# Kernel optimization log

Measured on AMD Instinct MI355X. Metric: run time of the kernel, lower is better.

## Reference

```python
import jax, jax.numpy as jnp
import numpy as np

N = 8192
E = 262144
IN_DIM = 128
OUT_DIM = 16


def _linear_params(key, fan_in, fan_out):
    k1, k2 = jax.random.split(key)
    bound = 1.0 / np.sqrt(fan_in)
    W = jax.random.uniform(k1, (fan_in, fan_out), jnp.float32, -bound, bound)
    b = jax.random.uniform(k2, (fan_out,), jnp.float32, -bound, bound)
    return W, b


def setup_inputs() -> dict:
    key = jax.random.key(0)
    ks = jax.random.split(key, 10)
    x = jax.random.normal(ks[0], (N, IN_DIM), jnp.float32)
    edge_index = jax.random.randint(ks[1], (2, E), 0, N, jnp.int64)
    W1, b1 = _linear_params(ks[2], IN_DIM, 128)
    W2, b2 = _linear_params(ks[3], 128, 256)
    W3, b3 = _linear_params(ks[4], 256, 64)
    Wk, bk = _linear_params(ks[5], 256, 256)
    Wq, bq = _linear_params(ks[6], 256, 256)
    Wr, br = _linear_params(ks[7], IN_DIM, 64)
    Wf, bf = _linear_params(ks[8], 64, OUT_DIM)
    ln_g = jnp.ones((64,), jnp.float32)
    ln_b = jnp.zeros((64,), jnp.float32)
    return dict(x=x, edge_index=edge_index, W1=W1, b1=b1, W2=W2, b2=b2,
                W3=W3, b3=b3, Wk=Wk, bk=bk, Wq=Wq, bq=bq, Wr=Wr, br=br,
                ln_g=ln_g, ln_b=ln_b, Wf=Wf, bf=bf)


def gcn_conv(x, W, b, row, col, n):
    # PyG GCNConv: add self-loops, symmetric normalization, aggregate src->dst
    xw = x @ W                                          # [N, F_out]
    loops = jnp.arange(n, dtype=row.dtype)
    r = jnp.concatenate([row, loops])
    c = jnp.concatenate([col, loops])
    deg = jax.ops.segment_sum(jnp.ones_like(c, jnp.float32), c, num_segments=n)
    dinv = jnp.where(deg > 0, jax.lax.rsqrt(jnp.maximum(deg, 1e-12)), 0.0)
    norm = dinv[r] * dinv[c]                            # [E+N]
    out = jax.ops.segment_sum(norm[:, None] * xw[r], c, num_segments=n)
    return out + b


def _forward(x, edge_index, W1, b1, W2, b2, W3, b3, Wk, bk, Wq, bq,
             Wr, br, ln_g, ln_b, Wf, bf):
    row, col = edge_index[0], edge_index[1]
    n = x.shape[0]
    residual = x @ Wr + br                              # [N, 64]
    h = jax.nn.leaky_relu(gcn_conv(x, W1, b1, row, col, n))   # dropout = eval no-op
    h = jax.nn.leaky_relu(gcn_conv(h, W2, b2, row, col, n))   # [N, 256]
    keys = h @ Wk + bk
    queries = h @ Wq + bq
    scores = queries @ keys.T                           # [N, N] dense, as in source
    mask = jnp.zeros((n, n), jnp.float32).at[row, col].set(1.0)
    scores = scores * mask                              # multiplicative mask (faithful)
    attn = jax.nn.softmax(scores, axis=-1)
    h = attn @ h                                        # [N, 256]
    h = jax.nn.leaky_relu(gcn_conv(h, W3, b3, row, col, n))   # [N, 64]
    z = h + residual
    mu = jnp.mean(z, axis=-1, keepdims=True)
    var = jnp.mean((z - mu) ** 2, axis=-1, keepdims=True)
    z = (z - mu) * jax.lax.rsqrt(var + 1e-5) * ln_g + ln_b
    pooled = jnp.max(z, axis=0)                         # 'max' pooling -> [64]
    return pooled @ Wf + bf                             # [OUT_DIM]


def reference(x, edge_index, W1, b1, W2, b2, W3, b3, Wk, bk, Wq, bq,
              Wr, br, ln_g, ln_b, Wf, bf):
    return _forward(x, edge_index, W1, b1, W2, b2, W3, b3, Wk, bk, Wq, bq,
                    Wr, br, ln_g, ln_b, Wf, bf)
```

## Files before the change

kernel.cpp:

```cpp
#include <hip/hip_runtime.h>
#include <hip/hip_fp16.h>
#include <cstdint>
#include <cstddef>

#define NNODES 8192
#define NEDGES 262144
#define MAXDEG 96
#define SMEM_BYTES 10496

typedef _Float16 f16x8 __attribute__((ext_vector_type(8)));
typedef _Float16 h2v   __attribute__((ext_vector_type(2)));
typedef float    f32x4 __attribute__((ext_vector_type(4)));

__device__ __forceinline__ float leaky(float v){ return v > 0.f ? v : 0.01f*v; }

__device__ __forceinline__ unsigned fmap(float f){
  unsigned u = __float_as_uint(f);
  return (u & 0x80000000u) ? ~u : (u | 0x80000000u);
}
__device__ __forceinline__ float funmap(unsigned u){
  return (u & 0x80000000u) ? __uint_as_float(u & 0x7FFFFFFFu) : __uint_as_float(~u);
}
__device__ __forceinline__ h2v as_h2(unsigned u){
  union{ unsigned x; h2v h; } c; c.x = u; return c.h;
}

struct GP {
  const float *x; const int *ei;
  const float *W1,*b1,*W2,*b2,*W3,*b3,*Wk,*bk,*Wq,*bq,*Wr,*br,*lng,*lnb,*Wf,*bfv;
  float* out;
  __half *xw1h,*h1h,*h1ah,*h2h,*qth,*gh,*hw3h;
  float *resid,*sw3;
  __half *Wqkt,*W2t,*W3t;
  float *bqk,*wb,*s0p;
  int *degc,*degr,*csrc,*csrd;
  unsigned* poolpart;
};

__device__ __forceinline__ void gemm_tile(const __half* __restrict__ A,
    const __half* __restrict__ Bt, const float* __restrict__ bias,
    float* __restrict__ Cf, __half* __restrict__ Ch, float* __restrict__ csum,
    int K, int N, int act, int bx, int by,
    _Float16 (*As)[40], _Float16 (*Bs)[40], float* cs){
  int t = threadIdx.x, w = t>>6, lane = t&63;
  int m0 = bx*64, n0 = by*64;
  int quad = lane>>4, l15 = lane&15;
  int srow = t>>2, soff = (t&3)*8;
  f32x4 acc0 = {0.f,0.f,0.f,0.f}, acc1 = acc0, acc2 = acc0, acc3 = acc0;
  for (int k0 = 0; k0 < K; k0 += 32){
    *(uint4*)&As[srow][soff] = *(const uint4*)(A  + (size_t)(m0+srow)*K + k0 + soff);
    *(uint4*)&Bs[srow][soff] = *(const uint4*)(Bt + (size_t)(n0+srow)*K + k0 + soff);
    __syncthreads();
    f16x8 af = *(const f16x8*)&As[w*16 + l15][quad*8];
    f16x8 b0 = *(const f16x8*)&Bs[ 0 + l15][quad*8];
    f16x8 b1 = *(const f16x8*)&Bs[16 + l15][quad*8];
    f16x8 b2 = *(const f16x8*)&Bs[32 + l15][quad*8];
    f16x8 b3 = *(const f16x8*)&Bs[48 + l15][quad*8];
    acc0 = __builtin_amdgcn_mfma_f32_16x16x32_f16(af, b0, acc0, 0,0,0);
    acc1 = __builtin_amdgcn_mfma_f32_16x16x32_f16(af, b1, acc1, 0,0,0);
    acc2 = __builtin_amdgcn_mfma_f32_16x16x32_f16(af, b2, acc2, 0,0,0);
    acc3 = __builtin_amdgcn_mfma_f32_16x16x32_f16(af, b3, acc3, 0,0,0);
    __syncthreads();
  }
  f32x4 accs[4] = {acc0, acc1, acc2, acc3};
  if (csum){
    if (t < 64) cs[t] = 0.f;
    __syncthreads();
    #pragma unroll
    for (int nt=0; nt<4; ++nt){
      float pp = accs[nt][0]+accs[nt][1]+accs[nt][2]+accs[nt][3];
      atomicAdd(&cs[nt*16 + l15], pp);
    }
    __syncthreads();
    if (t < 64) atomicAdd(&csum[n0 + t], cs[t]);
  }
  #pragma unroll
  for (int nt=0; nt<4; ++nt){
    int col = n0 + nt*16 + l15;
    float bv = bias ? bias[col] : 0.f;
    #pragma unroll
    for (int r=0;r<4;r++){
      int row = m0 + w*16 + quad*4 + r;
      float v = accs[nt][r] + bv;
      if (act) v = leaky(v);
      if (Cf) Cf[(size_t)row*N + col] = v;
      if (Ch) Ch[(size_t)row*N + col] = __float2half(v);
    }
  }
}

template<int TRANSB>
__device__ __forceinline__ void gemm_f32(const float* __restrict__ A,
    const float* __restrict__ B, const float* __restrict__ bias,
    float* __restrict__ Cf, __half* __restrict__ Ch,
    int K, int N, int bx, int by,
    _Float16 (*As)[40], _Float16 (*Bs)[40]){
  int t = threadIdx.x, w = t>>6, lane = t&63;
  int m0 = bx*64, n0 = by*64;
  int quad = lane>>4, l15 = lane&15;
  int srow = t>>2, soff = (t&3)*8;
  f32x4 acc0 = {0.f,0.f,0.f,0.f}, acc1 = acc0, acc2 = acc0, acc3 = acc0;
  for (int k0 = 0; k0 < K; k0 += 32){
    float4 a0 = *(const float4*)(A + (size_t)(m0+srow)*K + k0 + soff);
    float4 a1 = *(const float4*)(A + (size_t)(m0+srow)*K + k0 + soff + 4);
    _Float16* ad = &As[srow][soff];
    ad[0]=(_Float16)a0.x; ad[1]=(_Float16)a0.y; ad[2]=(_Float16)a0.z; ad[3]=(_Float16)a0.w;
    ad[4]=(_Float16)a1.x; ad[5]=(_Float16)a1.y; ad[6]=(_Float16)a1.z; ad[7]=(_Float16)a1.w;
    _Float16* bd = &Bs[srow][soff];
    if (TRANSB){
      #pragma unroll
      for (int u=0;u<8;u++)
        bd[u] = (_Float16)B[(size_t)(k0+soff+u)*N + n0+srow];
    } else {
      float4 b0 = *(const float4*)(B + (size_t)(n0+srow)*K + k0 + soff);
      float4 b1 = *(const float4*)(B + (size_t)(n0+srow)*K + k0 + soff + 4);
      bd[0]=(_Float16)b0.x; bd[1]=(_Float16)b0.y; bd[2]=(_Float16)b0.z; bd[3]=(_Float16)b0.w;
      bd[4]=(_Float16)b1.x; bd[5]=(_Float16)b1.y; bd[6]=(_Float16)b1.z; bd[7]=(_Float16)b1.w;
    }
    __syncthreads();
    f16x8 af = *(const f16x8*)&As[w*16 + l15][quad*8];
    f16x8 b0 = *(const f16x8*)&Bs[ 0 + l15][quad*8];
    f16x8 b1 = *(const f16x8*)&Bs[16 + l15][quad*8];
    f16x8 b2 = *(const f16x8*)&Bs[32 + l15][quad*8];
    f16x8 b3 = *(const f16x8*)&Bs[48 + l15][quad*8];
    acc0 = __builtin_amdgcn_mfma_f32_16x16x32_f16(af, b0, acc0, 0,0,0);
    acc1 = __builtin_amdgcn_mfma_f32_16x16x32_f16(af, b1, acc1, 0,0,0);
    acc2 = __builtin_amdgcn_mfma_f32_16x16x32_f16(af, b2, acc2, 0,0,0);
    acc3 = __builtin_amdgcn_mfma_f32_16x16x32_f16(af, b3, acc3, 0,0,0);
    __syncthreads();
  }
  f32x4 accs[4] = {acc0, acc1, acc2, acc3};
  #pragma unroll
  for (int nt=0; nt<4; ++nt){
    int col = n0 + nt*16 + l15;
    float bv = bias ? bias[col] : 0.f;
    #pragma unroll
    for (int r=0;r<4;r++){
      int row = m0 + w*16 + quad*4 + r;
      float v = accs[nt][r] + bv;
      if (Cf) Cf[(size_t)row*N + col] = v;
      if (Ch) Ch[(size_t)row*N + col] = __float2half(v);
    }
  }
}

template<int INS, int OUTS, int ACT>
__device__ __forceinline__ void agg128w(const __half* __restrict__ in,
    const int* __restrict__ deg, const int* __restrict__ src,
    __half* __restrict__ outp, const float* __restrict__ bias, int i){
  int lane = threadIdx.x & 63;
  int dcc = deg[i];
  float dc = rsqrtf((float)(dcc+1));
  int e0 = i*MAXDEG, e1 = e0 + dcc;
  float2 acc = make_float2(0.f, 0.f);
  for (int eb = e0; eb < e1; eb += 8){
    int m = e1 - eb; if (m > 8) m = 8;
    int r[8];
    #pragma unroll
    for (int u=0;u<8;u++) r[u] = src[(u<m) ? eb+u : eb];
    __half2 hv[8]; float sc[8];
    #pragma unroll
    for (int u=0;u<8;u++){
      hv[u] = *(const __half2*)(in + (size_t)r[u]*128 + lane*2);
      sc[u] = INS ? 1.f : rsqrtf((float)(deg[r[u]]+1));
    }
    #pragma unroll
    for (int u=0;u<8;u++){
      if (u < m){
        float2 h = __half22float2(hv[u]);
        if (INS){ acc.x += h.x; acc.y += h.y; }
        else { acc.x = fmaf(sc[u], h.x, acc.x); acc.y = fmaf(sc[u], h.y, acc.y); }
      }
    }
  }
  float2 self = __half22float2(*(const __half2*)(in + (size_t)i*128 + lane*2));
  float ss = INS ? 1.f : dc;
  float ox = dc*(ss*self.x + acc.x);
  float oy = dc*(ss*self.y + acc.y);
  if (ACT){
    ox = leaky(ox + bias[lane*2]);
    oy = leaky(oy + bias[lane*2+1]);
  }
  if (OUTS){ ox *= dc; oy *= dc; }
  *(__half2*)(outp + (size_t)i*128 + lane*2) = __floats2half2_rn(ox, oy);
}

__device__ __forceinline__ void attn_unit(const GP& p, int u){
  const int n = NNODES;
  int w = threadIdx.x>>6, lane = threadIdx.x&63;
  int i = u*4 + w;
  int fo = lane*4;
  uint2 qtu = *(const uint2*)(p.qth + (size_t)i*256 + fo);
  h2v q0 = as_h2(qtu.x), q1 = as_h2(qtu.y);
  float4 wbv = *(const float4*)(p.wb + fo);
  uint2 hiu  = *(const uint2*)(p.h2h + (size_t)i*256 + fo);
  float2 hia = __half22float2(*(__half2*)&hiu.x);
  float2 hib = __half22float2(*(__half2*)&hiu.y);
  float pv = hia.x*wbv.x + hia.y*wbv.y + hib.x*wbv.z + hib.y*wbv.w;
  #pragma unroll
  for (int mm=32; mm; mm>>=1) pv += __shfl_xor(pv, mm, 64);
  float base = pv + p.s0p[0];
  int dri = p.degr[i];
  int e0 = i*MAXDEG, e1 = e0 + dri;
  float acc = 0.f, dsum = 0.f;
  int slot = lane & 7;
  for (int eb = e0; eb < e1; eb += 8){
    int m = e1 - eb; if (m > 8) m = 8;
    int j[8];
    #pragma unroll
    for (int u8=0;u8<8;u8++) j[u8] = p.csrd[(u8<m) ? eb+u8 : eb];
    uint2 hv[8]; float gv[8];
    #pragma unroll
    for (int u8=0;u8<8;u8++){
      hv[u8] = *(const uint2*)(p.h2h + (size_t)j[u8]*256 + fo);
      gv[u8] = __half2float(p.gh[(size_t)j[u8]*64 + lane]);
    }
    float d[8];
    #pragma unroll
    for (int u8=0;u8<8;u8++)
      d[u8] = __builtin_amdgcn_fdot2(q1, as_h2(hv[u8].y),
              __builtin_amdgcn_fdot2(q0, as_h2(hv[u8].x), 0.f, false), false);
    #pragma unroll
    for (int v=0;v<8;v++) d[v] += __shfl_xor(d[v], 1, 64);
    float e0_ = (lane&1) ? d[1] : d[0];
    float e1_ = (lane&1) ? d[3] : d[2];
    float e2_ = (lane&1) ? d[5] : d[4];
    float e3_ = (lane&1) ? d[7] : d[6];
    e0_ += __shfl_xor(e0_, 2, 64);  e1_ += __shfl_xor(e1_, 2, 64);
    e2_ += __shfl_xor(e2_, 2, 64);  e3_ += __shfl_xor(e3_, 2, 64);
    float f0_ = (lane&2) ? e1_ : e0_;
    float f1_ = (lane&2) ? e3_ : e2_;
    f0_ += __shfl_xor(f0_, 4, 64);  f1_ += __shfl_xor(f1_, 4, 64);
    float g_ = (lane&4) ? f1_ : f0_;
    g_ += __shfl_xor(g_,  8, 64);
    g_ += __shfl_xor(g_, 16, 64);
    g_ += __shfl_xor(g_, 32, 64);
    float wep = __expf(g_ + base);
    float wm = (slot < m) ? wep : 0.f;
    wm += __shfl_xor(wm, 1, 64);
    wm += __shfl_xor(wm, 2, 64);
    wm += __shfl_xor(wm, 4, 64);
    dsum += wm;
    #pragma unroll
    for (int u8=0;u8<8;u8++){
      if (u8 < m){
        float wu = __shfl(wep, u8, 64);
        acc = fmaf(wu - 1.f, gv[u8], acc);
      }
    }
  }
  float inv = 1.0f / ((float)(n - dri) + dsum);
  float di = rsqrtf((float)(p.degc[i]+1));
  p.hw3h[(size_t)i*64 + lane] = __float2half(di * (p.sw3[lane] + acc) * inv);
}

__device__ __forceinline__ void zp_wave(const GP& p, int c){
  int lane = threadIdx.x & 63;
  int dcc = p.degc[c];
  float dc = rsqrtf((float)(dcc+1));
  float acc = 0.f;
  int e0 = c*MAXDEG, e1 = e0 + dcc;
  for (int eb = e0; eb < e1; eb += 8){
    int m = e1 - eb; if (m > 8) m = 8;
    int r[8];
    #pragma unroll
    for (int u=0;u<8;u++) r[u] = p.csrc[(u<m) ? eb+u : eb];
    __half hval[8];
    #pragma unroll
    for (int u=0;u<8;u++) hval[u] = p.hw3h[(size_t)r[u]*64 + lane];
    #pragma unroll
    for (int u=0;u<8;u++)
      if (u < m) acc += __half2float(hval[u]);
  }
  float self = __half2float(p.hw3h[(size_t)c*64 + lane]);
  float v = leaky(dc*(self + acc) + p.b3[lane]) + p.resid[(size_t)c*64 + lane];
  float s = v;
  #pragma unroll
  for (int mm=32; mm; mm>>=1) s += __shfl_xor(s, mm, 64);
  float mu = s * (1.0f/64.0f);
  float d = v - mu;
  float s2 = d*d;
  #pragma unroll
  for (int mm=32; mm; mm>>=1) s2 += __shfl_xor(s2, mm, 64);
  float zv = d * rsqrtf(s2*(1.0f/64.0f) + 1e-5f) * p.lng[lane] + p.lnb[lane];
  atomicMax(&p.poolpart[(c & 63)*64 + lane], fmap(zv));
}

__device__ __forceinline__ void final_unit(const GP& p, char* smem){
  int t = threadIdx.x, f = t & 63, g = t >> 6;
  unsigned (*sm)[64] = (unsigned(*)[64])smem;
  float* pool = (float*)(smem + 1024);
  unsigned mu = 0u;
  for (int b = g; b < 64; b += 4) mu = max(mu, p.poolpart[b*64 + f]);
  sm[g][f] = mu;
  __syncthreads();
  if (g == 0)
    pool[f] = funmap(max(max(sm[0][f],sm[1][f]), max(sm[2][f],sm[3][f])));
  __syncthreads();
  if (t < 16){
    float a = p.bfv[t];
    #pragma unroll
    for (int ff=0; ff<64; ++ff) a = fmaf(pool[ff], p.Wf[ff*16 + t], a);
    p.out[t] = a;
  }
}

__global__ __launch_bounds__(256) void k_z(GP p){
  __shared__ float smv[768];
  int b = blockIdx.x, t = threadIdx.x;
  if (b < 16){
    int idx = b*256 + t;
    int4 z = {0,0,0,0};
    ((int4*)p.degc)[idx] = z;
  } else if (b < 144){
    int idx = (b-16)*256 + t;
    int nn = idx >> 7, k = idx & 127;
    p.W2t[idx] = __float2half(p.W2[k*256 + nn]);
  } else if (b < 208){
    int idx = (b-144)*256 + t;
    int nn = idx >> 8, k = idx & 255;
    p.W3t[idx] = __float2half(p.W3[k*64 + nn]);
  } else if (b < 224){
    p.poolpart[(b-208)*256 + t] = 0u;
  } else if (b == 224){
    if (t < 64) p.sw3[t] = 0.f;
  } else {
    int c = b - 225;
    float* ra = smv; float* rb = smv + 256; float* rc = smv + 512;
    ra[t] = p.Wk[c*256 + t] * p.bq[t];
    rb[t] = p.Wq[c*256 + t] * p.bk[t];
    if (c == 0) rc[t] = p.bq[t]*p.bk[t];
    __syncthreads();
    for (int off=128; off; off>>=1){
      if (t < off){
        ra[t] += ra[t+off];
        rb[t] += rb[t+off];
        if (c == 0) rc[t] += rc[t+off];
      }
      __syncthreads();
    }
    if (t == 0){
      p.bqk[c] = ra[0];
      p.wb[c]  = rb[0];
      if (c == 0) p.s0p[0] = rc[0];
    }
  }
}

__global__ __launch_bounds__(256) void k_pre(GP p){
  __shared__ __align__(16) char smem[SMEM_BYTES];
  _Float16 (*As)[40] = (_Float16(*)[40])smem;
  _Float16 (*Bs)[40] = (_Float16(*)[40])(smem + 5120);
  int b = blockIdx.x, t = threadIdx.x;
  if (b < 1024){
    int e = b*256 + t;
    int r = p.ei[e], c = p.ei[NEDGES+e];
    int p1 = atomicAdd(&p.degc[c],1); p.csrc[c*MAXDEG + p1] = r;
    int p2 = atomicAdd(&p.degr[r],1); p.csrd[r*MAXDEG + p2] = c;
  } else if (b < 1280){
    int bb = b - 1024;
    gemm_f32<1>(p.x, p.W1, nullptr, nullptr, p.xw1h, 128, 128, bb>>1, bb&1, As, Bs);
  } else if (b < 1296){
    int bb = b - 1280;
    gemm_f32<0>(p.Wk, p.Wq, nullptr, nullptr, p.Wqkt, 256, 256, bb&3, bb>>2, As, Bs);
  } else {
    gemm_f32<1>(p.x, p.Wr, p.br, p.resid, nullptr, 128, 64, b-1296, 0, As, Bs);
  }
}

__global__ __launch_bounds__(256) void k_agg0(GP p){
  int i = blockIdx.x*4 + (threadIdx.x>>6);
  agg128w<0,1,1>(p.xw1h, p.degc, p.csrc, p.h1h, p.b1, i);
}
__global__ __launch_bounds__(256) void k_agg1(GP p){
  int i = blockIdx.x*4 + (threadIdx.x>>6);
  agg128w<1,0,0>(p.h1h, p.degc, p.csrc, p.h1ah, nullptr, i);
}

__global__ __launch_bounds__(256) void k_gemm2(GP p){
  __shared__ __align__(16) char smem[SMEM_BYTES];
  _Float16 (*As)[40] = (_Float16(*)[40])smem;
  _Float16 (*Bs)[40] = (_Float16(*)[40])(smem + 5120);
  int b = blockIdx.x;
  gemm_tile(p.h1ah, p.W2t, p.b2, nullptr, p.h2h, nullptr, 128, 256, 1, b>>2, b&3, As, Bs, nullptr);
}

__global__ __launch_bounds__(256) void k_mix2(GP p){
  __shared__ __align__(16) char smem[SMEM_BYTES];
  _Float16 (*As)[40] = (_Float16(*)[40])smem;
  _Float16 (*Bs)[40] = (_Float16(*)[40])(smem + 5120);
  float* cs = (float*)(smem + 10240);
  int b = blockIdx.x;
  if (b < 128) gemm_tile(p.h2h, p.W3t, nullptr, nullptr, p.gh, p.sw3, 256, 64, 0, b, 0, As, Bs, cs);
  else {
    int bb = b - 128;
    gemm_tile(p.h2h, p.Wqkt, p.bqk, nullptr, p.qth, nullptr, 256, 256, 0, bb>>2, bb&3, As, Bs, cs);
  }
}

__global__ __launch_bounds__(256) void k_attn(GP p){ attn_unit(p, blockIdx.x); }

__global__ __launch_bounds__(256) void k_zp(GP p){
  int c = blockIdx.x*4 + (threadIdx.x>>6);
  zp_wave(p, c);
}

__global__ __launch_bounds__(256) void k_final(GP p){
  __shared__ __align__(16) char smem[SMEM_BYTES];
  final_unit(p, smem);
}

extern "C" void kernel_launch(void* const* d_in, const int* in_sizes, int n_in,
                              void* d_out, int out_size, void* d_ws, size_t ws_size,
                              hipStream_t stream){
  const int n = NNODES, E = NEDGES;
  char* ws = (char*)d_ws; size_t off = 0;
  auto alloc = [&](size_t bytes)->void*{
    void* pp = ws + off; off += (bytes + 255) & ~(size_t)255; return pp;
  };
  GP p;
  p.x   = (const float*)d_in[0];
  p.ei  = (const int*)d_in[1];
  p.W1  = (const float*)d_in[2];  p.b1 = (const float*)d_in[3];
  p.W2  = (const float*)d_in[4];  p.b2 = (const float*)d_in[5];
  p.W3  = (const float*)d_in[6];  p.b3 = (const float*)d_in[7];
  p.Wk  = (const float*)d_in[8];  p.bk = (const float*)d_in[9];
  p.Wq  = (const float*)d_in[10]; p.bq = (const float*)d_in[11];
  p.Wr  = (const float*)d_in[12]; p.br = (const float*)d_in[13];
  p.lng = (const float*)d_in[14]; p.lnb = (const float*)d_in[15];
  p.Wf  = (const float*)d_in[16]; p.bfv = (const float*)d_in[17];
  p.out = (float*)d_out;

  p.degc = (int*)alloc((size_t)n*4);
  p.degr = (int*)alloc((size_t)n*4);
  p.xw1h = (__half*)alloc((size_t)n*128*2);
  p.h1h  = (__half*)alloc((size_t)n*128*2);
  p.h1ah = (__half*)alloc((size_t)n*128*2);
  p.h2h  = (__half*)alloc((size_t)n*256*2);
  p.qth  = (__half*)alloc((size_t)n*256*2);
  p.gh   = (__half*)alloc((size_t)n*64*2);
  p.hw3h = (__half*)alloc((size_t)n*64*2);
  p.resid= (float*)alloc((size_t)n*64*4);
  p.sw3  = (float*)alloc(64*4);
  p.Wqkt = (__half*)alloc(256*256*2);
  p.W2t  = (__half*)alloc(128*256*2);
  p.W3t  = (__half*)alloc(256*64*2);
  p.bqk  = (float*)alloc(256*4);
  p.wb   = (float*)alloc(256*4);
  p.s0p  = (float*)alloc(4);
  p.csrc = (int*)alloc((size_t)n*MAXDEG*4);
  p.csrd = (int*)alloc((size_t)n*MAXDEG*4);
  p.poolpart = (unsigned*)alloc(64*64*4);

  k_z    <<<dim3(481),  256, 0, stream>>>(p);
  k_pre  <<<dim3(1424), 256, 0, stream>>>(p);
  k_agg0 <<<dim3(n/4),  256, 0, stream>>>(p);
  k_agg1 <<<dim3(n/4),  256, 0, stream>>>(p);
  k_gemm2<<<dim3(512),  256, 0, stream>>>(p);
  k_mix2 <<<dim3(640),  256, 0, stream>>>(p);
  k_attn <<<dim3(n/4),  256, 0, stream>>>(p);
  k_zp   <<<dim3(n/4),  256, 0, stream>>>(p);
  k_final<<<dim3(1),    256, 0, stream>>>(p);
}
```

Before: 203.3 us.

## Fuse W2 GEMM with Q/K and W3 GEMMs into one row-block kernel

Replaces the two launches k_gemm2 and k_mix2 with a single kernel, k_gm. Each block owns 16 rows: it computes h2 = leaky(h1a·W2 + b2), keeps that h2 tile in shared memory, and immediately multiplies it by Wqk and W3. This removes one kernel launch and avoids re-reading h2 from global memory for the second-stage GEMMs. In exchange, every block re-streams the full weight matrices for only 16 rows, and the grid has 512 blocks of smaller tiles, which may lower MFMA efficiency and raise L2 weight traffic.

```diff
diff --git a/kernel.cpp b/kernel.cpp
--- a/kernel.cpp
+++ b/kernel.cpp
@@ -36,58 +36,6 @@
   int *degc,*degr,*csrc,*csrd;
   unsigned* poolpart;
 };
-
-__device__ __forceinline__ void gemm_tile(const __half* __restrict__ A,
-    const __half* __restrict__ Bt, const float* __restrict__ bias,
-    float* __restrict__ Cf, __half* __restrict__ Ch, float* __restrict__ csum,
-    int K, int N, int act, int bx, int by,
-    _Float16 (*As)[40], _Float16 (*Bs)[40], float* cs){
-  int t = threadIdx.x, w = t>>6, lane = t&63;
-  int m0 = bx*64, n0 = by*64;
-  int quad = lane>>4, l15 = lane&15;
-  int srow = t>>2, soff = (t&3)*8;
-  f32x4 acc0 = {0.f,0.f,0.f,0.f}, acc1 = acc0, acc2 = acc0, acc3 = acc0;
-  for (int k0 = 0; k0 < K; k0 += 32){
-    *(uint4*)&As[srow][soff] = *(const uint4*)(A  + (size_t)(m0+srow)*K + k0 + soff);
-    *(uint4*)&Bs[srow][soff] = *(const uint4*)(Bt + (size_t)(n0+srow)*K + k0 + soff);
-    __syncthreads();
-    f16x8 af = *(const f16x8*)&As[w*16 + l15][quad*8];
-    f16x8 b0 = *(const f16x8*)&Bs[ 0 + l15][quad*8];
-    f16x8 b1 = *(const f16x8*)&Bs[16 + l15][quad*8];
-    f16x8 b2 = *(const f16x8*)&Bs[32 + l15][quad*8];
-    f16x8 b3 = *(const f16x8*)&Bs[48 + l15][quad*8];
-    acc0 = __builtin_amdgcn_mfma_f32_16x16x32_f16(af, b0, acc0, 0,0,0);
-    acc1 = __builtin_amdgcn_mfma_f32_16x16x32_f16(af, b1, acc1, 0,0,0);
-    acc2 = __builtin_amdgcn_mfma_f32_16x16x32_f16(af, b2, acc2, 0,0,0);
-    acc3 = __builtin_amdgcn_mfma_f32_16x16x32_f16(af, b3, acc3, 0,0,0);
-    __syncthreads();
-  }
-  f32x4 accs[4] = {acc0, acc1, acc2, acc3};
-  if (csum){
-    if (t < 64) cs[t] = 0.f;
-    __syncthreads();
-    #pragma unroll
-    for (int nt=0; nt<4; ++nt){
-      float pp = accs[nt][0]+accs[nt][1]+accs[nt][2]+accs[nt][3];
-      atomicAdd(&cs[nt*16 + l15], pp);
-    }
-    __syncthreads();
-    if (t < 64) atomicAdd(&csum[n0 + t], cs[t]);
-  }
-  #pragma unroll
-  for (int nt=0; nt<4; ++nt){
-    int col = n0 + nt*16 + l15;
-    float bv = bias ? bias[col] : 0.f;
-    #pragma unroll
-    for (int r=0;r<4;r++){
-      int row = m0 + w*16 + quad*4 + r;
-      float v = accs[nt][r] + bv;
-      if (act) v = leaky(v);
-      if (Cf) Cf[(size_t)row*N + col] = v;
-      if (Ch) Ch[(size_t)row*N + col] = __float2half(v);
-    }
-  }
-}
 
 template<int TRANSB>
 __device__ __forceinline__ void gemm_f32(const float* __restrict__ A,
@@ -377,24 +325,96 @@
   agg128w<1,0,0>(p.h1h, p.degc, p.csrc, p.h1ah, nullptr, i);
 }
 
-__global__ __launch_bounds__(256) void k_gemm2(GP p){
-  __shared__ __align__(16) char smem[SMEM_BYTES];
-  _Float16 (*As)[40] = (_Float16(*)[40])smem;
-  _Float16 (*Bs)[40] = (_Float16(*)[40])(smem + 5120);
-  int b = blockIdx.x;
-  gemm_tile(p.h1ah, p.W2t, p.b2, nullptr, p.h2h, nullptr, 128, 256, 1, b>>2, b&3, As, Bs, nullptr);
-}
-
-__global__ __launch_bounds__(256) void k_mix2(GP p){
-  __shared__ __align__(16) char smem[SMEM_BYTES];
-  _Float16 (*As)[40] = (_Float16(*)[40])smem;
-  _Float16 (*Bs)[40] = (_Float16(*)[40])(smem + 5120);
-  float* cs = (float*)(smem + 10240);
-  int b = blockIdx.x;
-  if (b < 128) gemm_tile(p.h2h, p.W3t, nullptr, nullptr, p.gh, p.sw3, 256, 64, 0, b, 0, As, Bs, cs);
-  else {
-    int bb = b - 128;
-    gemm_tile(p.h2h, p.Wqkt, p.bqk, nullptr, p.qth, nullptr, 256, 256, 0, bb>>2, bb&3, As, Bs, cs);
+__global__ __launch_bounds__(256) void k_gm(GP p){
+  __shared__ _Float16 h1a[16][136];
+  __shared__ _Float16 h2s[16][264];
+  __shared__ _Float16 BsQ[256][40];
+  __shared__ _Float16 BsG[64][40];
+  __shared__ float cs[64];
+  int t = threadIdx.x, w = t>>6, lane = t&63;
+  int quad = lane>>4, l15 = lane&15;
+  int base = blockIdx.x*16;
+  int soff = (t&3)*8, srow4 = t>>2;
+  {
+    int r = t>>4, c0 = (t&15)*8;
+    *(uint4*)&h1a[r][c0] = *(const uint4*)(p.h1ah + (size_t)(base+r)*128 + c0);
+  }
+  if (t < 64) cs[t] = 0.f;
+  f32x4 a1[4];
+  #pragma unroll
+  for (int nt=0;nt<4;++nt) a1[nt] = (f32x4){0.f,0.f,0.f,0.f};
+  for (int k0=0;k0<128;k0+=32){
+    __syncthreads();
+    #pragma unroll
+    for (int pp=0;pp<4;pp++){
+      int row = pp*64 + srow4;
+      *(uint4*)&BsQ[row][soff] = *(const uint4*)(p.W2t + (size_t)row*128 + k0 + soff);
+    }
+    __syncthreads();
+    f16x8 af = *(const f16x8*)&h1a[l15][k0 + quad*8];
+    #pragma unroll
+    for (int nt=0;nt<4;++nt){
+      f16x8 bf = *(const f16x8*)&BsQ[w*64 + nt*16 + l15][quad*8];
+      a1[nt] = __builtin_amdgcn_mfma_f32_16x16x32_f16(af, bf, a1[nt], 0,0,0);
+    }
+  }
+  __syncthreads();
+  #pragma unroll
+  for (int nt=0;nt<4;++nt){
+    int col = w*64 + nt*16 + l15;
+    float bv = p.b2[col];
+    #pragma unroll
+    for (int r=0;r<4;r++){
+      int row = quad*4 + r;
+      float v = leaky(a1[nt][r] + bv);
+      __half h = __float2half(v);
+      h2s[row][col] = *(_Float16*)&h;
+      p.h2h[(size_t)(base+row)*256 + col] = h;
+    }
+  }
+  __syncthreads();
+  f32x4 aq[4]; f32x4 ag = (f32x4){0.f,0.f,0.f,0.f};
+  #pragma unroll
+  for (int nt=0;nt<4;++nt) aq[nt] = (f32x4){0.f,0.f,0.f,0.f};
+  for (int k0=0;k0<256;k0+=32){
+    #pragma unroll
+    for (int pp=0;pp<4;pp++){
+      int row = pp*64 + srow4;
+      *(uint4*)&BsQ[row][soff] = *(const uint4*)(p.Wqkt + (size_t)row*256 + k0 + soff);
+    }
+    *(uint4*)&BsG[srow4][soff] = *(const uint4*)(p.W3t + (size_t)srow4*256 + k0 + soff);
+    __syncthreads();
+    f16x8 af = *(const f16x8*)&h2s[l15][k0 + quad*8];
+    #pragma unroll
+    for (int nt=0;nt<4;++nt){
+      f16x8 bf = *(const f16x8*)&BsQ[w*64 + nt*16 + l15][quad*8];
+      aq[nt] = __builtin_amdgcn_mfma_f32_16x16x32_f16(af, bf, aq[nt], 0,0,0);
+    }
+    f16x8 bg = *(const f16x8*)&BsG[w*16 + l15][quad*8];
+    ag = __builtin_amdgcn_mfma_f32_16x16x32_f16(af, bg, ag, 0,0,0);
+    __syncthreads();
+  }
+  #pragma unroll
+  for (int nt=0;nt<4;++nt){
+    int col = w*64 + nt*16 + l15;
+    float bv = p.bqk[col];
+    #pragma unroll
+    for (int r=0;r<4;r++){
+      int row = quad*4 + r;
+      p.qth[(size_t)(base+row)*256 + col] = __float2half(aq[nt][r] + bv);
+    }
+  }
+  {
+    int col = w*16 + l15;
+    float partial = ag[0]+ag[1]+ag[2]+ag[3];
+    #pragma unroll
+    for (int r=0;r<4;r++){
+      int row = quad*4 + r;
+      p.gh[(size_t)(base+row)*64 + col] = __float2half(ag[r]);
+    }
+    atomicAdd(&cs[col], partial);
+    __syncthreads();
+    if (t < 64) atomicAdd(&p.sw3[t], cs[t]);
   }
 }
 
@@ -456,8 +476,7 @@
   k_pre  <<<dim3(1424), 256, 0, stream>>>(p);
   k_agg0 <<<dim3(n/4),  256, 0, stream>>>(p);
   k_agg1 <<<dim3(n/4),  256, 0, stream>>>(p);
-  k_gemm2<<<dim3(512),  256, 0, stream>>>(p);
-  k_mix2 <<<dim3(640),  256, 0, stream>>>(p);
+  k_gm   <<<dim3(n/16), 256, 0, stream>>>(p);
   k_attn <<<dim3(n/4),  256, 0, stream>>>(p);
   k_zp   <<<dim3(n/4),  256, 0, stream>>>(p);
   k_final<<<dim3(1),    256, 0, stream>>>(p);
```

Result: slower. 213.3 us (+4.9%).
